# Optimization experiments

Hardware: AMD Instinct MI355X
Metric: run time of the kernel (lower is better)

## Reference

```python
import jax, jax.numpy as jnp
import numpy as np

B = 262144
HID = 256
HEADS = 8


def setup_inputs() -> dict:
    key = jax.random.key(0)
    ks = jax.random.split(key, 8)
    s = 1.0 / np.sqrt(HID)
    return {
        "fine_messages": jax.random.normal(ks[0], (B, HID), jnp.float32),
        "coarse_messages": jax.random.normal(ks[1], (B, HID), jnp.float32),
        "motif_features": jax.random.normal(ks[2], (B, HID), jnp.float32),
        "Wq": jax.random.normal(ks[3], (HID, HID), jnp.float32) * s,
        "Wk": jax.random.normal(ks[4], (HID, HID), jnp.float32) * s,
        "Wv": jax.random.normal(ks[5], (HID, HID), jnp.float32) * s,
        "Wo": jax.random.normal(ks[6], (HID, HID), jnp.float32) * s,
        "bo": jax.random.normal(ks[7], (HID,), jnp.float32) * s,
        "heads": HEADS,
    }


def reference(fine_messages, coarse_messages, motif_features, Wq, Wk, Wv, Wo, bo, heads):
    b, hid = motif_features.shape
    d_k = hid // heads
    # K/V share the same pre-projection input: [fine; coarse] -> (B, 2, hid)
    kv_in = jnp.stack([fine_messages, coarse_messages], axis=1)
    # torch Linear(x) = x @ W.T (no bias on q/k/v projections)
    q = (motif_features @ Wq.T).reshape(b, heads, d_k)          # (B, H, d_k) single query
    k = (kv_in @ Wk.T).reshape(b, 2, heads, d_k)                # (B, 2, H, d_k)
    v = (kv_in @ Wv.T).reshape(b, 2, heads, d_k)
    # NOTE: original divides by d_k, not sqrt(d_k)
    scores = jnp.einsum("bhd,bshd->bhs", q, k) / d_k            # (B, H, 2)
    att = jax.nn.softmax(scores, axis=-1)
    out = jnp.einsum("bhs,bshd->bhd", att, v).reshape(b, hid)   # (B, hid)
    return out @ Wo.T + bo
```

## Files before the change

### kernel.cpp

```cpp
#include <hip/hip_runtime.h>

#define B_TOT 262144
#define HID   256
#define NHEAD 8
#define BR    64
#define NTHR  256

typedef __bf16 bf16_t;
typedef __attribute__((ext_vector_type(8))) __bf16 bf16x8;
typedef __attribute__((ext_vector_type(4))) __bf16 bf16x4;
typedef __attribute__((ext_vector_type(4))) float  f32x4;

#define QKV_BYTES (384 * 1024)

static __device__ __forceinline__ f32x4 mfma16(bf16x8 a, bf16x8 b, f32x4 c) {
  return __builtin_amdgcn_mfma_f32_16x16x32_bf16(a, b, c, 0, 0, 0);
}

static __device__ __forceinline__ bf16x8 cvt8(float4 a, float4 b) {
  bf16x8 r;
  r[0] = (bf16_t)a.x; r[1] = (bf16_t)a.y; r[2] = (bf16_t)a.z; r[3] = (bf16_t)a.w;
  r[4] = (bf16_t)b.x; r[5] = (bf16_t)b.y; r[6] = (bf16_t)b.z; r[7] = (bf16_t)b.w;
  return r;
}

static __device__ __forceinline__ bf16x8 pin8(bf16x8 v) {
  f32x4 t = __builtin_bit_cast(f32x4, v);
  asm volatile("" : "+v"(t));
  return __builtin_bit_cast(bf16x8, t);
}

typedef __attribute__((address_space(3))) void lds_void;
typedef __attribute__((address_space(1))) void gbl_void;
static __device__ __forceinline__ void gload_lds16(const void* g, void* l) {
  __builtin_amdgcn_global_load_lds((gbl_void*)g, (lds_void*)l, 16, 0, 0);
}

__global__ __launch_bounds__(256) void pack_weights(
    const float* __restrict__ Wq, const float* __restrict__ Wk,
    const float* __restrict__ Wv, const float* __restrict__ Wo,
    bf16_t* __restrict__ ws) {
  const int t     = blockIdx.x * 256 + threadIdx.x;
  const int lane  = t & 63;
  const int chunk = t >> 6;
  const int l15 = lane & 15, lg = lane >> 4;
  const float* src;
  int row, col;
  if (chunk < 384) {
    const int slot = chunk % 6;
    const int hk   = chunk / 6;
    const int wi = slot >> 1, half = slot & 1;
    const int h = hk >> 3, ks = hk & 7;
    src = (wi == 0) ? Wq : (wi == 1) ? Wk : Wv;
    row = h * 32 + (l15 >> 2) * 8 + half * 4 + (l15 & 3);
    col = ks * 32 + lg * 8;
  } else {
    const int c  = chunk - 384;
    const int ks = c >> 4, jt = c & 15;
    src = Wo;
    row = jt * 16 + l15;
    col = ks * 32 + lg * 8;
  }
  const float* p = src + (size_t)row * HID + col;
  const float4 a = *(const float4*)p;
  const float4 b = *(const float4*)(p + 4);
  *(bf16x8*)(ws + (size_t)t * 8) = cvt8(a, b);
}

__global__ __launch_bounds__(NTHR, 2) void fused_local_aug(
    const float* __restrict__ fine, const float* __restrict__ coarse,
    const float* __restrict__ motif, const bf16_t* __restrict__ wpk,
    const float* __restrict__ bo, float* __restrict__ out) {
  __shared__ char wbuf[49152];

  const int tid  = threadIdx.x;
  const int lane = tid & 63;
  const int wave = tid >> 6;
  const int l15  = lane & 15;
  const int lg   = lane >> 4;
  const size_t row0 = (size_t)blockIdx.x * BR;
  const size_t mrow = row0 + wave * 16 + l15;

  bf16x8 xm[8], xf[8], xc[8];
  {
    const float* pm = motif  + mrow * HID + lg * 8;
    const float* pf = fine   + mrow * HID + lg * 8;
    const float* pc = coarse + mrow * HID + lg * 8;
#pragma unroll
    for (int s = 0; s < 8; ++s) {
      xm[s] = pin8(cvt8(*(const float4*)(pm + s * 32), *(const float4*)(pm + s * 32 + 4)));
      xf[s] = pin8(cvt8(*(const float4*)(pf + s * 32), *(const float4*)(pf + s * 32 + 4)));
      xc[s] = pin8(cvt8(*(const float4*)(pc + s * 32), *(const float4*)(pc + s * 32 + 4)));
    }
  }

  bf16x4 mo0[NHEAD], mo1[NHEAD];

#pragma unroll
  for (int h = 0; h < NHEAD; ++h) {
    __syncthreads();
#pragma unroll
    for (int i = 0; i < 12; ++i)
      gload_lds16((const char*)wpk + h * 49152 + i * 4096 + tid * 16,
                  wbuf + i * 4096 + tid * 16);
    __syncthreads();

    f32x4 aQ0{}, aQ1{}, aK10{}, aK11{}, aK20{}, aK21{}, aV10{}, aV11{}, aV20{}, aV21{};
#pragma unroll
    for (int ks = 0; ks < 8; ++ks) {
      const char* p = wbuf + ks * 6144 + lane * 16;
      bf16x8 q0 = *(const bf16x8*)(p);
      bf16x8 q1 = *(const bf16x8*)(p + 1024);
      bf16x8 k0 = *(const bf16x8*)(p + 2048);
      bf16x8 k1 = *(const bf16x8*)(p + 3072);
      bf16x8 v0 = *(const bf16x8*)(p + 4096);
      bf16x8 v1 = *(const bf16x8*)(p + 5120);
      aQ0  = mfma16(q0, xm[ks], aQ0);   aQ1  = mfma16(q1, xm[ks], aQ1);
      aK10 = mfma16(k0, xf[ks], aK10);  aK11 = mfma16(k1, xf[ks], aK11);
      aK20 = mfma16(k0, xc[ks], aK20);  aK21 = mfma16(k1, xc[ks], aK21);
      aV10 = mfma16(v0, xf[ks], aV10);  aV11 = mfma16(v1, xf[ks], aV11);
      aV20 = mfma16(v0, xc[ks], aV20);  aV21 = mfma16(v1, xc[ks], aV21);
    }
    float s1 = 0.f, s2 = 0.f;
#pragma unroll
    for (int r = 0; r < 4; ++r) {
      s1 += aQ0[r] * aK10[r] + aQ1[r] * aK11[r];
      s2 += aQ0[r] * aK20[r] + aQ1[r] * aK21[r];
    }
    s1 += __shfl_xor(s1, 16); s1 += __shfl_xor(s1, 32);
    s2 += __shfl_xor(s2, 16); s2 += __shfl_xor(s2, 32);
    s1 *= (1.0f / 32.0f);  s2 *= (1.0f / 32.0f);
    const float mx = fmaxf(s1, s2);
    const float e1 = __expf(s1 - mx), e2 = __expf(s2 - mx);
    const float a1 = e1 / (e1 + e2);
    const float a2 = 1.0f - a1;
#pragma unroll
    for (int r = 0; r < 4; ++r) {
      mo0[h][r] = (bf16_t)(a1 * aV10[r] + a2 * aV20[r]);
      mo1[h][r] = (bf16_t)(a1 * aV11[r] + a2 * aV21[r]);
    }
  }

  bf16x8 mfrag[NHEAD];
#pragma unroll
  for (int h = 0; h < NHEAD; ++h) {
    bf16x8 t;
    t[0] = mo0[h][0]; t[1] = mo0[h][1]; t[2] = mo0[h][2]; t[3] = mo0[h][3];
    t[4] = mo1[h][0]; t[5] = mo1[h][1]; t[6] = mo1[h][2]; t[7] = mo1[h][3];
    mfrag[h] = t;
  }

  f32x4 acc[16];
#pragma unroll
  for (int jt = 0; jt < 16; ++jt) acc[jt] = f32x4{0.f, 0.f, 0.f, 0.f};

#pragma unroll
  for (int p = 0; p < 4; ++p) {
    __syncthreads();
#pragma unroll
    for (int i = 0; i < 8; ++i)
      gload_lds16((const char*)wpk + QKV_BYTES + p * 32768 + i * 4096 + tid * 16,
                  wbuf + i * 4096 + tid * 16);
    __syncthreads();
#pragma unroll
    for (int ksl = 0; ksl < 2; ++ksl) {
      bf16x8 mf = mfrag[p * 2 + ksl];
      const char* pb = wbuf + ksl * 16384 + lane * 16;
#pragma unroll
      for (int jt = 0; jt < 16; ++jt) {
        bf16x8 wf = *(const bf16x8*)(pb + jt * 1024);
        acc[jt] = mfma16(wf, mf, acc[jt]);
      }
    }
  }

#pragma unroll
  for (int jt = 0; jt < 16; ++jt) {
    const int jj = jt * 16 + lg * 4;
    const float4 b4 = *(const float4*)(bo + jj);
    f32x4 o;
    o[0] = acc[jt][0] + b4.x;
    o[1] = acc[jt][1] + b4.y;
    o[2] = acc[jt][2] + b4.z;
    o[3] = acc[jt][3] + b4.w;
    __builtin_nontemporal_store(o, (f32x4*)(out + mrow * HID + jj));
  }
}

extern "C" void kernel_launch(void* const* d_in, const int* in_sizes, int n_in,
                              void* d_out, int out_size, void* d_ws, size_t ws_size,
                              hipStream_t stream) {
  (void)in_sizes; (void)n_in; (void)ws_size; (void)out_size;
  const float* fine   = (const float*)d_in[0];
  const float* coarse = (const float*)d_in[1];
  const float* motif  = (const float*)d_in[2];
  const float* Wq     = (const float*)d_in[3];
  const float* Wk     = (const float*)d_in[4];
  const float* Wv     = (const float*)d_in[5];
  const float* Wo     = (const float*)d_in[6];
  const float* bo     = (const float*)d_in[7];
  float* out          = (float*)d_out;
  bf16_t* wpk         = (bf16_t*)d_ws;

  pack_weights<<<128, 256, 0, stream>>>(Wq, Wk, Wv, Wo, wpk);
  fused_local_aug<<<B_TOT / BR, NTHR, 0, stream>>>(fine, coarse, motif, wpk, bo, out);
}
```

Measured before the change: 406.1 us.

## Double-buffer weight staging in LDS and double the rows per block

Weights are now staged into LDS in 24 KB halves through a two-slot ring. The next slice is issued before computing on the current one, so global-to-LDS copies overlap MFMA work and the load-then-sync before every head goes away. The first weight stage is also issued before the activation loads. The block grows to 128 rows and 512 threads. The launch bound now asks for 6 blocks per CU, which may squeeze the register budget and cause spills of the large register-resident activation fragments.

```diff
diff --git a/kernel.cpp b/kernel.cpp
--- a/kernel.cpp
+++ b/kernel.cpp
@@ -3,8 +3,8 @@
 #define B_TOT 262144
 #define HID   256
 #define NHEAD 8
-#define BR    64
-#define NTHR  256
+#define BR    128
+#define NTHR  512
 
 typedef __bf16 bf16_t;
 typedef __attribute__((ext_vector_type(8))) __bf16 bf16x8;
@@ -67,7 +67,7 @@
   *(bf16x8*)(ws + (size_t)t * 8) = cvt8(a, b);
 }
 
-__global__ __launch_bounds__(NTHR, 2) void fused_local_aug(
+__global__ __launch_bounds__(NTHR, 6) void fused_local_aug(
     const float* __restrict__ fine, const float* __restrict__ coarse,
     const float* __restrict__ motif, const bf16_t* __restrict__ wpk,
     const float* __restrict__ bo, float* __restrict__ out) {
@@ -81,6 +81,23 @@
   const size_t row0 = (size_t)blockIdx.x * BR;
   const size_t mrow = row0 + wave * 16 + l15;
 
+  auto stage = [&](int ph) {
+    if (ph >= 24) return;
+    char* dst = wbuf + (ph & 1) * 24576 + tid * 16;
+    if (ph < 16) {
+      const char* src = (const char*)wpk + (ph >> 1) * 49152 + (ph & 1) * 24576 + tid * 16;
+      gload_lds16(src, dst);
+      gload_lds16(src + 8192, dst + 8192);
+      gload_lds16(src + 16384, dst + 16384);
+    } else {
+      const char* src = (const char*)wpk + QKV_BYTES + (ph - 16) * 16384 + tid * 16;
+      gload_lds16(src, dst);
+      gload_lds16(src + 8192, dst + 8192);
+    }
+  };
+
+  stage(0);
+
   bf16x8 xm[8], xf[8], xc[8];
   {
     const float* pm = motif  + mrow * HID + lg * 8;
@@ -93,33 +110,34 @@
       xc[s] = pin8(cvt8(*(const float4*)(pc + s * 32), *(const float4*)(pc + s * 32 + 4)));
     }
   }
+  __syncthreads();
 
   bf16x4 mo0[NHEAD], mo1[NHEAD];
 
 #pragma unroll
   for (int h = 0; h < NHEAD; ++h) {
-    __syncthreads();
-#pragma unroll
-    for (int i = 0; i < 12; ++i)
-      gload_lds16((const char*)wpk + h * 49152 + i * 4096 + tid * 16,
-                  wbuf + i * 4096 + tid * 16);
-    __syncthreads();
-
     f32x4 aQ0{}, aQ1{}, aK10{}, aK11{}, aK20{}, aK21{}, aV10{}, aV11{}, aV20{}, aV21{};
 #pragma unroll
-    for (int ks = 0; ks < 8; ++ks) {
-      const char* p = wbuf + ks * 6144 + lane * 16;
-      bf16x8 q0 = *(const bf16x8*)(p);
-      bf16x8 q1 = *(const bf16x8*)(p + 1024);
-      bf16x8 k0 = *(const bf16x8*)(p + 2048);
-      bf16x8 k1 = *(const bf16x8*)(p + 3072);
-      bf16x8 v0 = *(const bf16x8*)(p + 4096);
-      bf16x8 v1 = *(const bf16x8*)(p + 5120);
-      aQ0  = mfma16(q0, xm[ks], aQ0);   aQ1  = mfma16(q1, xm[ks], aQ1);
-      aK10 = mfma16(k0, xf[ks], aK10);  aK11 = mfma16(k1, xf[ks], aK11);
-      aK20 = mfma16(k0, xc[ks], aK20);  aK21 = mfma16(k1, xc[ks], aK21);
-      aV10 = mfma16(v0, xf[ks], aV10);  aV11 = mfma16(v1, xf[ks], aV11);
-      aV20 = mfma16(v0, xc[ks], aV20);  aV21 = mfma16(v1, xc[ks], aV21);
+    for (int half = 0; half < 2; ++half) {
+      stage(2 * h + half + 1);
+      const char* pb = wbuf + ((2 * h + half) & 1) * 24576 + lane * 16;
+#pragma unroll
+      for (int kk = 0; kk < 4; ++kk) {
+        const int ks = half * 4 + kk;
+        const char* p = pb + kk * 6144;
+        bf16x8 q0 = *(const bf16x8*)(p);
+        bf16x8 q1 = *(const bf16x8*)(p + 1024);
+        bf16x8 k0 = *(const bf16x8*)(p + 2048);
+        bf16x8 k1 = *(const bf16x8*)(p + 3072);
+        bf16x8 v0 = *(const bf16x8*)(p + 4096);
+        bf16x8 v1 = *(const bf16x8*)(p + 5120);
+        aQ0  = mfma16(q0, xm[ks], aQ0);   aQ1  = mfma16(q1, xm[ks], aQ1);
+        aK10 = mfma16(k0, xf[ks], aK10);  aK11 = mfma16(k1, xf[ks], aK11);
+        aK20 = mfma16(k0, xc[ks], aK20);  aK21 = mfma16(k1, xc[ks], aK21);
+        aV10 = mfma16(v0, xf[ks], aV10);  aV11 = mfma16(v1, xf[ks], aV11);
+        aV20 = mfma16(v0, xc[ks], aV20);  aV21 = mfma16(v1, xc[ks], aV21);
+      }
+      __syncthreads();
     }
     float s1 = 0.f, s2 = 0.f;
 #pragma unroll
@@ -155,23 +173,16 @@
   for (int jt = 0; jt < 16; ++jt) acc[jt] = f32x4{0.f, 0.f, 0.f, 0.f};
 
 #pragma unroll
-  for (int p = 0; p < 4; ++p) {
+  for (int wp = 0; wp < 8; ++wp) {
+    stage(17 + wp);
+    bf16x8 mf = mfrag[wp];
+    const char* pb = wbuf + (wp & 1) * 24576 + lane * 16;
+#pragma unroll
+    for (int jt = 0; jt < 16; ++jt) {
+      bf16x8 wf = *(const bf16x8*)(pb + jt * 1024);
+      acc[jt] = mfma16(wf, mf, acc[jt]);
+    }
     __syncthreads();
-#pragma unroll
-    for (int i = 0; i < 8; ++i)
-      gload_lds16((const char*)wpk + QKV_BYTES + p * 32768 + i * 4096 + tid * 16,
-                  wbuf + i * 4096 + tid * 16);
-    __syncthreads();
-#pragma unroll
-    for (int ksl = 0; ksl < 2; ++ksl) {
-      bf16x8 mf = mfrag[p * 2 + ksl];
-      const char* pb = wbuf + ksl * 16384 + lane * 16;
-#pragma unroll
-      for (int jt = 0; jt < 16; ++jt) {
-        bf16x8 wf = *(const bf16x8*)(pb + jt * 1024);
-        acc[jt] = mfma16(wf, mf, acc[jt]);
-      }
-    }
   }
 
 #pragma unroll
```

Measured after the change: 1.189 ms. 193% more time.
